# Performance work log

Hardware: AMD Instinct MI355X
Metric: run time of the kernel (lower is better)

## Reference

```python
import jax, jax.numpy as jnp
import numpy as np

EMBED = 1024
HEADS = 16
B, T = 2, 1024


def setup_inputs() -> dict:
    key = jax.random.key(0)
    k1, k2 = jax.random.split(key)
    x = jax.random.normal(k1, (B, T, EMBED), dtype=jnp.float32)
    # causal mask: True positions are masked to -inf (torch masked_fill semantics)
    mask = jnp.triu(jnp.ones((T, T), dtype=bool), k=1)
    weight = jax.random.normal(k2, (HEADS * EMBED, EMBED), dtype=jnp.float32)
    return {"x": x, "mask": mask, "weight": weight}


def reference(x, mask, weight):
    b, t, c = x.shape
    h = weight.shape[0] // c  # num_heads
    # split channels into heads: (b, h, t, head_dim)
    y = x.reshape(b, t, h, c // h).transpose(0, 2, 1, 3)
    # per-head scores (b, h, t, t)
    s = jnp.einsum('bhtk,bhsk->bhts', y, y)
    # mask BEFORE scaling, then scale by sqrt(num_heads) (not head_dim!)
    s = jnp.where(mask, -jnp.inf, s)
    p = jax.nn.softmax(s / jnp.sqrt(jnp.asarray(h, dtype=s.dtype)), axis=-1)
    # V is raw x broadcast across heads: (b, h, t, c)
    o = jnp.einsum('bhts,bsc->bhtc', p, x)
    # concat heads -> (b, t, h*c), final linear
    o = o.transpose(0, 2, 1, 3).reshape(b, t, h * c)
    return o @ weight
```

## Files before the change

### kernel.cpp

```cpp
#include <hip/hip_runtime.h>
#include <hip/hip_bf16.h>

#define B_ 2
#define T_ 1024
#define C_ 1024
#define H_ 16

typedef short bf16x8 __attribute__((ext_vector_type(8)));
typedef float f32x4 __attribute__((ext_vector_type(4)));

#define MFMA16(a, b, c) __builtin_amdgcn_mfma_f32_16x16x32_bf16(a, b, c, 0, 0, 0)

__device__ inline short f2bf(float x) {
    union { __hip_bfloat16 h; short s; } u;
    u.h = __float2bfloat16(x);
    return u.s;
}

__device__ inline void gl_lds16(const void* g, void* l) {
    __builtin_amdgcn_global_load_lds(
        (const __attribute__((address_space(1))) unsigned int*)g,
        (__attribute__((address_space(3))) unsigned int*)l, 16, 0, 0);
}

__global__ __launch_bounds__(256) void cvt_x(const float* __restrict__ x,
                                             short* __restrict__ xb) {
    int idx = (blockIdx.x * 256 + threadIdx.x) * 8;
    float4 a = *(const float4*)(x + idx);
    float4 b = *(const float4*)(x + idx + 4);
    bf16x8 v;
    v[0] = f2bf(a.x); v[1] = f2bf(a.y); v[2] = f2bf(a.z); v[3] = f2bf(a.w);
    v[4] = f2bf(b.x); v[5] = f2bf(b.y); v[6] = f2bf(b.z); v[7] = f2bf(b.w);
    *(bf16x8*)(xb + idx) = v;
}

__global__ __launch_bounds__(256) void cvt_w(const float* __restrict__ W,
                                             short* __restrict__ Wt) {
    __shared__ float T[64][65];
    const int bid = blockIdx.x;
    const int nb = bid & 15, cb = (bid >> 4) & 15, h = bid >> 8;
    const int t = threadIdx.x;
    const int c0 = cb * 64, n0 = nb * 64;
    const float* src = W + (size_t)(h * 1024 + c0) * 1024 + n0;
    {
        const int cl = t >> 4, nl = (t & 15) * 4;
#pragma unroll
        for (int r = 0; r < 4; ++r) {
            float4 v = *(const float4*)(src + (size_t)(cl + r * 16) * 1024 + nl);
            T[cl + r * 16][nl + 0] = v.x;
            T[cl + r * 16][nl + 1] = v.y;
            T[cl + r * 16][nl + 2] = v.z;
            T[cl + r * 16][nl + 3] = v.w;
        }
    }
    __syncthreads();
    {
        short* dst = Wt + (size_t)(h * 1024 + n0) * 1024 + c0;
        const int nl = t >> 3, cl8 = (t & 7) * 8;
#pragma unroll
        for (int r = 0; r < 2; ++r) {
            const int n = nl + r * 32;
            bf16x8 o;
#pragma unroll
            for (int j = 0; j < 8; ++j) o[j] = f2bf(T[cl8 + j][n]);
            *(bf16x8*)(dst + (size_t)n * 1024 + cl8) = o;
        }
    }
}

__global__ __launch_bounds__(512, 2) void attn_po(const short* __restrict__ xb,
                                                  const short* __restrict__ xbT,
                                                  short* __restrict__ O) {
    __shared__ short Pb[2][64][72];
    __shared__ float row_al[2][64];
    __shared__ float row_l[64];
    __shared__ int   flags[2][4];

    const int tid = threadIdx.x;
    const int bh = blockIdx.x & 31;
    const int rest = blockIdx.x >> 5;
    const int tb = (rest < 8) ? rest : 23 - rest;
    const int b = bh >> 4, h = bh & 15;
    const int lane = tid & 63, q = lane >> 4, l16 = lane & 15;
    const int w = tid >> 6;
    const int g = w & 3;
    const int nw = w * 128;
    const short* xbb = xb + ((size_t)b << 20);
    const short* vtb = xbT + ((size_t)b << 20);

    const int t0 = tb * 64;
    const int nch = tb + 1;

    f32x4 acc[4][8];
#pragma unroll
    for (int mt = 0; mt < 4; ++mt)
#pragma unroll
        for (int nt = 0; nt < 8; ++nt) acc[mt][nt] = (f32x4){0.f, 0.f, 0.f, 0.f};
    float m_r[4], l_r[4];
#pragma unroll
    for (int r = 0; r < 4; ++r) { m_r[r] = -3.0e38f; l_r[r] = 0.f; }

    bf16x8 qf[2];
    if (w < 4) {
#pragma unroll
        for (int ks = 0; ks < 2; ++ks)
            qf[ks] = *(const bf16x8*)(xbb + (size_t)(t0 + g * 16 + l16) * 1024 +
                                      h * 64 + ks * 32 + q * 8);
    }

    for (int ci = -1; ci < nch; ++ci) {
        __syncthreads();
        const int cc = ci + 1;
        if (w < 4 && cc < nch) {
            const int s0 = (cc == 0) ? t0 : (cc - 1) * 64;
            const int par = cc & 1;
            f32x4 sf[4];
#pragma unroll
            for (int st = 0; st < 4; ++st) sf[st] = (f32x4){0.f, 0.f, 0.f, 0.f};
#pragma unroll
            for (int st = 0; st < 4; ++st)
#pragma unroll
                for (int ks = 0; ks < 2; ++ks) {
                    bf16x8 kf = *(const bf16x8*)(xbb +
                        (size_t)(s0 + st * 16 + l16) * 1024 + h * 64 + ks * 32 + q * 8);
                    sf[st] = MFMA16(qf[ks], kf, sf[st]);
                }
            float mx[4] = {-3.0e38f, -3.0e38f, -3.0e38f, -3.0e38f};
#pragma unroll
            for (int st = 0; st < 4; ++st)
#pragma unroll
                for (int r = 0; r < 4; ++r) {
                    float v = sf[st][r] * 0.25f;
                    if (cc == 0 && (s0 + st * 16 + l16) > (t0 + g * 16 + q * 4 + r))
                        v = -3.0e38f;
                    sf[st][r] = v;
                    mx[r] = fmaxf(mx[r], v);
                }
#pragma unroll
            for (int r = 0; r < 4; ++r) {
                mx[r] = fmaxf(mx[r], __shfl_xor(mx[r], 1));
                mx[r] = fmaxf(mx[r], __shfl_xor(mx[r], 2));
                mx[r] = fmaxf(mx[r], __shfl_xor(mx[r], 4));
                mx[r] = fmaxf(mx[r], __shfl_xor(mx[r], 8));
            }
            float sum[4], al[4];
            int upd = 0;
#pragma unroll
            for (int r = 0; r < 4; ++r) {
                float m_new = fmaxf(m_r[r], mx[r]);
                al[r] = __expf(m_r[r] - m_new);
                upd |= (m_new > m_r[r]) ? 1 : 0;
                m_r[r] = m_new;
                sum[r] = 0.f;
            }
#pragma unroll
            for (int st = 0; st < 4; ++st)
#pragma unroll
                for (int r = 0; r < 4; ++r) {
                    float pv = __expf(sf[st][r] - m_r[r]);
                    sum[r] += pv;
                    Pb[par][g * 16 + q * 4 + r][st * 16 + l16] = f2bf(pv);
                }
#pragma unroll
            for (int r = 0; r < 4; ++r) {
                sum[r] += __shfl_xor(sum[r], 1);
                sum[r] += __shfl_xor(sum[r], 2);
                sum[r] += __shfl_xor(sum[r], 4);
                sum[r] += __shfl_xor(sum[r], 8);
                l_r[r] = l_r[r] * al[r] + sum[r];
            }
            if (l16 == 0) {
#pragma unroll
                for (int r = 0; r < 4; ++r) row_al[par][g * 16 + q * 4 + r] = al[r];
            }
            int any_upd = __any(upd);
            if (lane == 0) flags[par][g] = any_upd;
        }
        if (ci >= 0) {
            const int par = ci & 1;
            if (flags[par][0] | flags[par][1] | flags[par][2] | flags[par][3]) {
#pragma unroll
                for (int mt = 0; mt < 4; ++mt) {
                    float a0 = row_al[par][mt * 16 + q * 4 + 0];
                    float a1 = row_al[par][mt * 16 + q * 4 + 1];
                    float a2 = row_al[par][mt * 16 + q * 4 + 2];
                    float a3 = row_al[par][mt * 16 + q * 4 + 3];
#pragma unroll
                    for (int nt = 0; nt < 8; ++nt) {
                        acc[mt][nt][0] *= a0;
                        acc[mt][nt][1] *= a1;
                        acc[mt][nt][2] *= a2;
                        acc[mt][nt][3] *= a3;
                    }
                }
            }
            bf16x8 pf[4][2];
#pragma unroll
            for (int mt = 0; mt < 4; ++mt)
#pragma unroll
                for (int ks = 0; ks < 2; ++ks)
                    pf[mt][ks] = *(bf16x8*)&Pb[par][mt * 16 + l16][ks * 32 + q * 8];
            const int s0p = (ci == 0) ? t0 : (ci - 1) * 64;
#pragma unroll
            for (int nt = 0; nt < 8; ++nt)
#pragma unroll
                for (int ks = 0; ks < 2; ++ks) {
                    bf16x8 vf = *(const bf16x8*)(vtb +
                        (size_t)(nw + nt * 16 + l16) * 1024 + s0p + ks * 32 + q * 8);
#pragma unroll
                    for (int mt = 0; mt < 4; ++mt)
                        acc[mt][nt] = MFMA16(pf[mt][ks], vf, acc[mt][nt]);
                }
        }
    }

    if (w < 4 && l16 == 0) {
#pragma unroll
        for (int r = 0; r < 4; ++r) row_l[g * 16 + q * 4 + r] = l_r[r];
    }
    __syncthreads();
    short* ob = O + ((((size_t)(b * 1024 + t0) * 16) + h) << 10);
#pragma unroll
    for (int mt = 0; mt < 4; ++mt) {
        float i0 = 1.f / row_l[mt * 16 + q * 4 + 0];
        float i1 = 1.f / row_l[mt * 16 + q * 4 + 1];
        float i2 = 1.f / row_l[mt * 16 + q * 4 + 2];
        float i3 = 1.f / row_l[mt * 16 + q * 4 + 3];
#pragma unroll
        for (int nt = 0; nt < 8; ++nt) {
            size_t base = (size_t)(mt * 16 + q * 4) * 16384 + nw + nt * 16 + l16;
            ob[base]         = f2bf(acc[mt][nt][0] * i0);
            ob[base + 16384] = f2bf(acc[mt][nt][1] * i1);
            ob[base + 32768] = f2bf(acc[mt][nt][2] * i2);
            ob[base + 49152] = f2bf(acc[mt][nt][3] * i3);
        }
    }
}

__global__ __launch_bounds__(256, 4) void ogemm(const short* __restrict__ O,
                                                const short* __restrict__ Wt,
                                                float* __restrict__ out) {
    __shared__ short Al[4][128][8];
    __shared__ short Bl[4][128][8];

    const int orig = blockIdx.x;
    const int x = orig & 7, j = orig >> 3;
    const int kq  = x >> 1;
    const int m_t = (x & 1) * 8 + (j >> 3);
    const int n_t = j & 7;
    const int m0 = m_t * 128, n0 = n_t * 128;
    const int t = threadIdx.x;
    const int lane = t & 63, q = lane >> 4, l16 = lane & 15;
    const int wv = t >> 6;
    const int wm = (wv & 1) * 64, wn = (wv >> 1) * 64;

    const short* Ab = O + (size_t)m0 * 16384;
    const int srow = t & 127, skg = t >> 7;

    char* al_base = (char*)&Al[0][0][0] + (size_t)t * 16;
    char* bl_base = (char*)&Bl[0][0][0] + (size_t)t * 16;

    f32x4 acc[4][4];
#pragma unroll
    for (int i = 0; i < 4; ++i)
#pragma unroll
        for (int j2 = 0; j2 < 4; ++j2) acc[i][j2] = (f32x4){0.f, 0.f, 0.f, 0.f};

    const int kbase = kq * 4096;
    for (int kk = 0; kk < 4096; kk += 32) {
        const int k0 = kbase + kk;
        const int h = k0 >> 10, c0 = k0 & 1023;
        const short* Bb = Wt + ((size_t)h << 20) + (size_t)n0 * 1024 + c0;
        __syncthreads();
        gl_lds16(Ab + (size_t)srow * 16384 + k0 + skg * 8, al_base);
        gl_lds16(Ab + (size_t)srow * 16384 + k0 + (skg + 2) * 8, al_base + 4096);
        gl_lds16(Bb + (size_t)srow * 1024 + skg * 8, bl_base);
        gl_lds16(Bb + (size_t)srow * 1024 + (skg + 2) * 8, bl_base + 4096);
        __syncthreads();
        bf16x8 af[4], bfr[4];
#pragma unroll
        for (int i = 0; i < 4; ++i) af[i] = *(bf16x8*)&Al[q][wm + i * 16 + l16][0];
#pragma unroll
        for (int j2 = 0; j2 < 4; ++j2) bfr[j2] = *(bf16x8*)&Bl[q][wn + j2 * 16 + l16][0];
#pragma unroll
        for (int i = 0; i < 4; ++i)
#pragma unroll
            for (int j2 = 0; j2 < 4; ++j2)
                acc[i][j2] = MFMA16(af[i], bfr[j2], acc[i][j2]);
    }

#pragma unroll
    for (int i = 0; i < 4; ++i)
#pragma unroll
        for (int j2 = 0; j2 < 4; ++j2)
#pragma unroll
            for (int r = 0; r < 4; ++r) {
                int m = m0 + wm + i * 16 + q * 4 + r;
                int n = n0 + wn + j2 * 16 + l16;
                atomicAdd(out + (size_t)m * 1024 + n, acc[i][j2][r]);
            }
}

__global__ __launch_bounds__(256, 4) void zgemm_fast(const short* __restrict__ xb,
                                                     const short* __restrict__ Wt,
                                                     short* __restrict__ ZT) {
    __shared__ short Al[4][128][8];
    __shared__ short Bl[4][128][8];

    const int bid = blockIdx.x;
    const int n_t = bid & 7, h = (bid >> 3) & 15, s_t = bid >> 7;
    const int n0 = n_t * 128, s0g = s_t * 128;
    const int t = threadIdx.x;
    const int lane = t & 63, q = lane >> 4, l16 = lane & 15;
    const int wv = t >> 6;
    const int wm = (wv & 1) * 64, wn = (wv >> 1) * 64;

    const short* Ab = Wt + ((size_t)h * 1024 + n0) * 1024;
    const short* Bb = xb + (size_t)s0g * 1024;
    const int srow = t & 127, skg = t >> 7;

    char* al_base = (char*)&Al[0][0][0] + (size_t)t * 16;
    char* bl_base = (char*)&Bl[0][0][0] + (size_t)t * 16;

    f32x4 acc[4][4];
#pragma unroll
    for (int i = 0; i < 4; ++i)
#pragma unroll
        for (int j = 0; j < 4; ++j) acc[i][j] = (f32x4){0.f, 0.f, 0.f, 0.f};

    for (int k0 = 0; k0 < 1024; k0 += 32) {
        __syncthreads();
        gl_lds16(Ab + (size_t)srow * 1024 + k0 + skg * 8, al_base);
        gl_lds16(Ab + (size_t)srow * 1024 + k0 + (skg + 2) * 8, al_base + 4096);
        gl_lds16(Bb + (size_t)srow * 1024 + k0 + skg * 8, bl_base);
        gl_lds16(Bb + (size_t)srow * 1024 + k0 + (skg + 2) * 8, bl_base + 4096);
        __syncthreads();
        bf16x8 af[4], bfr[4];
#pragma unroll
        for (int i = 0; i < 4; ++i) af[i] = *(bf16x8*)&Al[q][wm + i * 16 + l16][0];
#pragma unroll
        for (int j = 0; j < 4; ++j) bfr[j] = *(bf16x8*)&Bl[q][wn + j * 16 + l16][0];
#pragma unroll
        for (int i = 0; i < 4; ++i)
#pragma unroll
            for (int j = 0; j < 4; ++j)
                acc[i][j] = MFMA16(af[i], bfr[j], acc[i][j]);
    }

    const int b = s0g >> 10, s_in0 = s0g & 1023;
    short* zb = ZT + ((size_t)(b * 16 + h) << 20);
#pragma unroll
    for (int i = 0; i < 4; ++i)
#pragma unroll
        for (int j = 0; j < 4; ++j)
#pragma unroll
            for (int r = 0; r < 4; ++r) {
                int n = n0 + wm + i * 16 + q * 4 + r;
                int s = s_in0 + wn + j * 16 + l16;
                zb[(size_t)n * 1024 + s] = f2bf(acc[i][j][r]);
            }
}

#define ZPAD 40

__global__ __launch_bounds__(256, 2) void zgemm_sm(const short* __restrict__ xb,
                                                   const float* __restrict__ W,
                                                   short* __restrict__ ZT) {
    __shared__ short Wts[128 * ZPAD];
    __shared__ short Xs[2][128 * ZPAD];

    const int tid = threadIdx.x;
    const int bs = blockIdx.x & 7;
    const int bn = (blockIdx.x >> 3) & 7;
    const int h  = blockIdx.x >> 6;
    const int s0 = bs * 128, n0 = bn * 128;
    const int lane = tid & 63, q = lane >> 4, l16 = lane & 15;
    const int w = tid >> 6, bw = w >> 1, sh = w & 1;

    f32x4 acc[8][4];
#pragma unroll
    for (int i = 0; i < 8; ++i)
#pragma unroll
        for (int j = 0; j < 4; ++j) acc[i][j] = (f32x4){0.f, 0.f, 0.f, 0.f};

    for (int k0 = 0; k0 < 1024; k0 += 32) {
        __syncthreads();
#pragma unroll
        for (int r = 0; r < 2; ++r) {
            const int c2 = ((tid >> 5) << 1) + (r << 4);
            const float* w0p = W + (size_t)(h * 1024 + k0 + c2) * 1024 + n0;
            const float* w1p = w0p + 1024;
#pragma unroll
            for (int i = 0; i < 4; ++i) {
                const int n = (tid & 31) + (i << 5);
                float wa = w0p[n], wb = w1p[n];
                unsigned u = (unsigned)(unsigned short)f2bf(wa) |
                             ((unsigned)(unsigned short)f2bf(wb) << 16);
                *(unsigned*)&Wts[n * ZPAD + c2] = u;
            }
        }
#pragma unroll
        for (int i = 0; i < 4; ++i) {
            const int id = tid + (i << 8);
            const int b2 = id >> 9, s = (id >> 2) & 127, cg = id & 3;
            bf16x8 v = *(const bf16x8*)(xb + (size_t)b2 * (T_ * C_) +
                                        (size_t)(s0 + s) * 1024 + k0 + cg * 8);
            *(bf16x8*)&Xs[b2][s * ZPAD + cg * 8] = v;
        }
        __syncthreads();

        bf16x8 af[8], bfr[4];
#pragma unroll
        for (int nt = 0; nt < 8; ++nt)
            af[nt] = *(bf16x8*)&Wts[(nt * 16 + l16) * ZPAD + q * 8];
#pragma unroll
        for (int st = 0; st < 4; ++st)
            bfr[st] = *(bf16x8*)&Xs[bw][(sh * 64 + st * 16 + l16) * ZPAD + q * 8];
#pragma unroll
        for (int nt = 0; nt < 8; ++nt)
#pragma unroll
            for (int st = 0; st < 4; ++st)
                acc[nt][st] = MFMA16(af[nt], bfr[st], acc[nt][st]);
    }

    short* zb = ZT + (size_t)(bw * 16 + h) * (1024 * 1024);
#pragma unroll
    for (int nt = 0; nt < 8; ++nt)
#pragma unroll
        for (int st = 0; st < 4; ++st)
#pragma unroll
            for (int r = 0; r < 4; ++r) {
                int n_abs = n0 + nt * 16 + q * 4 + r;
                int s_abs = s0 + sh * 64 + st * 16 + l16;
                zb[(size_t)n_abs * 1024 + s_abs] = f2bf(acc[nt][st][r]);
            }
}

__global__ __launch_bounds__(512, 2) void attn(const short* __restrict__ xb,
                                               const short* __restrict__ ZT,
                                               float* __restrict__ out) {
    __shared__ short Pb[2][64][72];
    __shared__ float row_al[2][64];
    __shared__ float row_l[64];
    __shared__ int   flags[2][4];

    const int tid = threadIdx.x;
    const int bh = blockIdx.x & 31, p = blockIdx.x >> 5;
    const int b = bh >> 4, h = bh & 15;
    const int lane = tid & 63, q = lane >> 4, l16 = lane & 15;
    const int w = tid >> 6;
    const int g = w & 3;
    const int nw = w * 128;
    const short* xbb = xb + ((size_t)b << 20);
    const short* ztb = ZT + ((size_t)(b * 16 + h) << 20);

    const int tiles[2] = { p, 15 - p };
    for (int ti = 0; ti < 2; ++ti) {
        const int tb = tiles[ti];
        const int t0 = tb * 64;
        const int nch = tb + 1;

        f32x4 acc[4][8];
#pragma unroll
        for (int mt = 0; mt < 4; ++mt)
#pragma unroll
            for (int nt = 0; nt < 8; ++nt) acc[mt][nt] = (f32x4){0.f, 0.f, 0.f, 0.f};
        float m_r[4], l_r[4];
#pragma unroll
        for (int r = 0; r < 4; ++r) { m_r[r] = -3.0e38f; l_r[r] = 0.f; }

        bf16x8 qf[2];
        if (w < 4) {
#pragma unroll
            for (int ks = 0; ks < 2; ++ks)
                qf[ks] = *(const bf16x8*)(xbb + (size_t)(t0 + g * 16 + l16) * 1024 +
                                          h * 64 + ks * 32 + q * 8);
        }

        for (int ci = -1; ci < nch; ++ci) {
            __syncthreads();
            const int cc = ci + 1;
            if (w < 4 && cc < nch) {
                const int s0 = (cc == 0) ? t0 : (cc - 1) * 64;
                const int par = cc & 1;
                f32x4 sf[4];
#pragma unroll
                for (int st = 0; st < 4; ++st) sf[st] = (f32x4){0.f, 0.f, 0.f, 0.f};
#pragma unroll
                for (int st = 0; st < 4; ++st)
#pragma unroll
                    for (int ks = 0; ks < 2; ++ks) {
                        bf16x8 kf = *(const bf16x8*)(xbb +
                            (size_t)(s0 + st * 16 + l16) * 1024 + h * 64 + ks * 32 + q * 8);
                        sf[st] = MFMA16(qf[ks], kf, sf[st]);
                    }
                float mx[4] = {-3.0e38f, -3.0e38f, -3.0e38f, -3.0e38f};
#pragma unroll
                for (int st = 0; st < 4; ++st)
#pragma unroll
                    for (int r = 0; r < 4; ++r) {
                        float v = sf[st][r] * 0.25f;
                        if (cc == 0 && (s0 + st * 16 + l16) > (t0 + g * 16 + q * 4 + r))
                            v = -3.0e38f;
                        sf[st][r] = v;
                        mx[r] = fmaxf(mx[r], v);
                    }
#pragma unroll
                for (int r = 0; r < 4; ++r) {
                    mx[r] = fmaxf(mx[r], __shfl_xor(mx[r], 1));
                    mx[r] = fmaxf(mx[r], __shfl_xor(mx[r], 2));
                    mx[r] = fmaxf(mx[r], __shfl_xor(mx[r], 4));
                    mx[r] = fmaxf(mx[r], __shfl_xor(mx[r], 8));
                }
                float sum[4], al[4];
                int upd = 0;
#pragma unroll
                for (int r = 0; r < 4; ++r) {
                    float m_new = fmaxf(m_r[r], mx[r]);
                    al[r] = __expf(m_r[r] - m_new);
                    upd |= (m_new > m_r[r]) ? 1 : 0;
                    m_r[r] = m_new;
                    sum[r] = 0.f;
                }
#pragma unroll
                for (int st = 0; st < 4; ++st)
#pragma unroll
                    for (int r = 0; r < 4; ++r) {
                        float pv = __expf(sf[st][r] - m_r[r]);
                        sum[r] += pv;
                        Pb[par][g * 16 + q * 4 + r][st * 16 + l16] = f2bf(pv);
                    }
#pragma unroll
                for (int r = 0; r < 4; ++r) {
                    sum[r] += __shfl_xor(sum[r], 1);
                    sum[r] += __shfl_xor(sum[r], 2);
                    sum[r] += __shfl_xor(sum[r], 4);
                    sum[r] += __shfl_xor(sum[r], 8);
                    l_r[r] = l_r[r] * al[r] + sum[r];
                }
                if (l16 == 0) {
#pragma unroll
                    for (int r = 0; r < 4; ++r) row_al[par][g * 16 + q * 4 + r] = al[r];
                }
                int any_upd = __any(upd);
                if (lane == 0) flags[par][g] = any_upd;
            }
            if (ci >= 0) {
                const int par = ci & 1;
                if (flags[par][0] | flags[par][1] | flags[par][2] | flags[par][3]) {
#pragma unroll
                    for (int mt = 0; mt < 4; ++mt) {
                        float a0 = row_al[par][mt * 16 + q * 4 + 0];
                        float a1 = row_al[par][mt * 16 + q * 4 + 1];
                        float a2 = row_al[par][mt * 16 + q * 4 + 2];
                        float a3 = row_al[par][mt * 16 + q * 4 + 3];
#pragma unroll
                        for (int nt = 0; nt < 8; ++nt) {
                            acc[mt][nt][0] *= a0;
                            acc[mt][nt][1] *= a1;
                            acc[mt][nt][2] *= a2;
                            acc[mt][nt][3] *= a3;
                        }
                    }
                }
                bf16x8 pf[4][2];
#pragma unroll
                for (int mt = 0; mt < 4; ++mt)
#pragma unroll
                    for (int ks = 0; ks < 2; ++ks)
                        pf[mt][ks] = *(bf16x8*)&Pb[par][mt * 16 + l16][ks * 32 + q * 8];
                const int s0p = (ci == 0) ? t0 : (ci - 1) * 64;
#pragma unroll
                for (int nt = 0; nt < 8; ++nt)
#pragma unroll
                    for (int ks = 0; ks < 2; ++ks) {
                        bf16x8 vf = *(const bf16x8*)(ztb +
                            (size_t)(nw + nt * 16 + l16) * 1024 + s0p + ks * 32 + q * 8);
#pragma unroll
                        for (int mt = 0; mt < 4; ++mt)
                            acc[mt][nt] = MFMA16(pf[mt][ks], vf, acc[mt][nt]);
                    }
            }
        }

        if (w < 4 && l16 == 0) {
#pragma unroll
            for (int r = 0; r < 4; ++r) row_l[g * 16 + q * 4 + r] = l_r[r];
        }
        __syncthreads();
#pragma unroll
        for (int mt = 0; mt < 4; ++mt) {
            float i0 = 1.f / row_l[mt * 16 + q * 4 + 0];
            float i1 = 1.f / row_l[mt * 16 + q * 4 + 1];
            float i2 = 1.f / row_l[mt * 16 + q * 4 + 2];
            float i3 = 1.f / row_l[mt * 16 + q * 4 + 3];
#pragma unroll
            for (int nt = 0; nt < 8; ++nt) {
                size_t base = (size_t)(b * 1024 + t0 + mt * 16 + q * 4) * 1024 +
                              nw + nt * 16 + l16;
                atomicAdd(out + base,            acc[mt][nt][0] * i0);
                atomicAdd(out + base + 1024,     acc[mt][nt][1] * i1);
                atomicAdd(out + base + 2048,     acc[mt][nt][2] * i2);
                atomicAdd(out + base + 3072,     acc[mt][nt][3] * i3);
            }
        }
        __syncthreads();
    }
}

extern "C" void kernel_launch(void* const* d_in, const int* in_sizes, int n_in,
                              void* d_out, int out_size, void* d_ws, size_t ws_size,
                              hipStream_t stream) {
    const float* x = (const float*)d_in[0];
    const float* W = (const float*)d_in[2];
    float* out = (float*)d_out;

    hipMemsetAsync(d_out, 0, (size_t)B_ * T_ * C_ * sizeof(float), stream);

    if (ws_size >= (size_t)104 * 1024 * 1024) {
        short* xb  = (short*)d_ws;
        short* xbT = xb + (size_t)2 * 1024 * 1024;
        short* Wt  = xb + (size_t)4 * 1024 * 1024;
        short* O   = xb + (size_t)20 * 1024 * 1024;

        cvt_x<<<(B_ * T_ * C_) / (256 * 8), 256, 0, stream>>>(x, xb);
        cvt_w<<<B_ * 16 * 16, 256, 0, stream>>>(x, xbT);
        cvt_w<<<16 * 16 * 16, 256, 0, stream>>>(W, Wt);
        attn_po<<<512, 512, 0, stream>>>(xb, xbT, O);
        ogemm<<<4 * 16 * 8, 256, 0, stream>>>(O, Wt, out);
    } else {
        short* xb = (short*)d_ws;
        short* ZT = (short*)d_ws + (size_t)B_ * T_ * C_;
        short* Wt = ZT + (size_t)B_ * H_ * 1024 * 1024;

        const bool big_ws = ws_size >= (size_t)100 * 1024 * 1024;
        cvt_x<<<(B_ * T_ * C_) / (256 * 8), 256, 0, stream>>>(x, xb);
        if (big_ws) {
            cvt_w<<<16 * 16 * 16, 256, 0, stream>>>(W, Wt);
            zgemm_fast<<<16 * 16 * 8, 256, 0, stream>>>(xb, Wt, ZT);
        } else {
            zgemm_sm<<<H_ * 8 * 8, 256, 0, stream>>>(xb, W, ZT);
        }
        attn<<<256, 512, 0, stream>>>(xb, ZT, out);
    }
}
```

Before: 355.2 us.

## Double-buffer LDS in ogemm with 64-wide K steps to overlap loads and MFMA

The output-projection GEMM now uses two LDS buffers, each holding a 64-wide K slice. The global-to-LDS loads for the next slice are issued before the MFMAs on the current slice run, and each step needs only one barrier instead of two. This is meant to hide global load latency and halve the synchronization overhead. LDS use per block goes up fourfold, so launch bounds drop to two blocks per CU, which lowers occupancy.

```diff
diff --git a/kernel.cpp b/kernel.cpp
--- a/kernel.cpp
+++ b/kernel.cpp
@@ -237,11 +237,13 @@
     }
 }
 
-__global__ __launch_bounds__(256, 4) void ogemm(const short* __restrict__ O,
+__global__ __launch_bounds__(256, 2) void ogemm(const short* __restrict__ O,
                                                 const short* __restrict__ Wt,
                                                 float* __restrict__ out) {
-    __shared__ short Al[4][128][8];
-    __shared__ short Bl[4][128][8];
+    __shared__ short Al0[8][128][8];
+    __shared__ short Bl0[8][128][8];
+    __shared__ short Al1[8][128][8];
+    __shared__ short Bl1[8][128][8];
 
     const int orig = blockIdx.x;
     const int x = orig & 7, j = orig >> 3;
@@ -257,8 +259,10 @@
     const short* Ab = O + (size_t)m0 * 16384;
     const int srow = t & 127, skg = t >> 7;
 
-    char* al_base = (char*)&Al[0][0][0] + (size_t)t * 16;
-    char* bl_base = (char*)&Bl[0][0][0] + (size_t)t * 16;
+    char* a0 = (char*)&Al0[0][0][0] + (size_t)t * 16;
+    char* b0 = (char*)&Bl0[0][0][0] + (size_t)t * 16;
+    char* a1 = (char*)&Al1[0][0][0] + (size_t)t * 16;
+    char* b1 = (char*)&Bl1[0][0][0] + (size_t)t * 16;
 
     f32x4 acc[4][4];
 #pragma unroll
@@ -267,27 +271,55 @@
         for (int j2 = 0; j2 < 4; ++j2) acc[i][j2] = (f32x4){0.f, 0.f, 0.f, 0.f};
 
     const int kbase = kq * 4096;
-    for (int kk = 0; kk < 4096; kk += 32) {
-        const int k0 = kbase + kk;
-        const int h = k0 >> 10, c0 = k0 & 1023;
-        const short* Bb = Wt + ((size_t)h << 20) + (size_t)n0 * 1024 + c0;
-        __syncthreads();
-        gl_lds16(Ab + (size_t)srow * 16384 + k0 + skg * 8, al_base);
-        gl_lds16(Ab + (size_t)srow * 16384 + k0 + (skg + 2) * 8, al_base + 4096);
-        gl_lds16(Bb + (size_t)srow * 1024 + skg * 8, bl_base);
-        gl_lds16(Bb + (size_t)srow * 1024 + (skg + 2) * 8, bl_base + 4096);
-        __syncthreads();
-        bf16x8 af[4], bfr[4];
-#pragma unroll
-        for (int i = 0; i < 4; ++i) af[i] = *(bf16x8*)&Al[q][wm + i * 16 + l16][0];
-#pragma unroll
-        for (int j2 = 0; j2 < 4; ++j2) bfr[j2] = *(bf16x8*)&Bl[q][wn + j2 * 16 + l16][0];
-#pragma unroll
-        for (int i = 0; i < 4; ++i)
-#pragma unroll
-            for (int j2 = 0; j2 < 4; ++j2)
-                acc[i][j2] = MFMA16(af[i], bfr[j2], acc[i][j2]);
-    }
+
+#define OG_STAGE(K0, AB, BB)                                                   \
+    {                                                                          \
+        const int k0_ = (K0);                                                  \
+        const int h_ = k0_ >> 10, c0_ = k0_ & 1023;                            \
+        const short* Arow_ = Ab + (size_t)srow * 16384 + k0_;                  \
+        const short* Brow_ = Wt + ((size_t)h_ << 20) +                         \
+                             (size_t)(n0 + srow) * 1024 + c0_;                 \
+        _Pragma("unroll")                                                      \
+        for (int jj = 0; jj < 4; ++jj) {                                       \
+            gl_lds16(Arow_ + (2 * jj + skg) * 8, (AB) + jj * 4096);            \
+            gl_lds16(Brow_ + (2 * jj + skg) * 8, (BB) + jj * 4096);            \
+        }                                                                      \
+    }
+
+#define OG_COMPUTE(ALARR, BLARR)                                               \
+    _Pragma("unroll")                                                          \
+    for (int ks = 0; ks < 2; ++ks) {                                           \
+        bf16x8 af[4], bfr[4];                                                  \
+        _Pragma("unroll")                                                      \
+        for (int i = 0; i < 4; ++i)                                            \
+            af[i] = *(bf16x8*)&ALARR[q + 4 * ks][wm + i * 16 + l16][0];        \
+        _Pragma("unroll")                                                      \
+        for (int j2 = 0; j2 < 4; ++j2)                                         \
+            bfr[j2] = *(bf16x8*)&BLARR[q + 4 * ks][wn + j2 * 16 + l16][0];     \
+        _Pragma("unroll")                                                      \
+        for (int i = 0; i < 4; ++i)                                            \
+            _Pragma("unroll")                                                  \
+            for (int j2 = 0; j2 < 4; ++j2)                                     \
+                acc[i][j2] = MFMA16(af[i], bfr[j2], acc[i][j2]);               \
+    }
+
+    OG_STAGE(kbase, a0, b0);
+    asm volatile("s_waitcnt vmcnt(0)" ::: "memory");
+    __builtin_amdgcn_s_barrier();
+
+    for (int kk = 0; kk < 4096; kk += 128) {
+        OG_STAGE(kbase + kk + 64, a1, b1);
+        OG_COMPUTE(Al0, Bl0);
+        asm volatile("s_waitcnt vmcnt(0)" ::: "memory");
+        __builtin_amdgcn_s_barrier();
+
+        if (kk + 128 < 4096) OG_STAGE(kbase + kk + 128, a0, b0);
+        OG_COMPUTE(Al1, Bl1);
+        asm volatile("s_waitcnt vmcnt(0)" ::: "memory");
+        __builtin_amdgcn_s_barrier();
+    }
+#undef OG_STAGE
+#undef OG_COMPUTE
 
 #pragma unroll
     for (int i = 0; i < 4; ++i)
@@ -627,7 +659,7 @@
         cvt_w<<<B_ * 16 * 16, 256, 0, stream>>>(x, xbT);
         cvt_w<<<16 * 16 * 16, 256, 0, stream>>>(W, Wt);
         attn_po<<<512, 512, 0, stream>>>(xb, xbT, O);
-        ogemm<<<4 * 16 * 8, 256, 0, stream>>>(O, Wt, out);
+        ogemm<<<512, 256, 0, stream>>>(O, Wt, out);
     } else {
         short* xb = (short*)d_ws;
         short* ZT = (short*)d_ws + (size_t)B_ * T_ * C_;
```

Result: slower. 384.5 us (+8.2%).
